# Kernel tuning notes

Hardware: AMD Instinct MI355X
Metric: run time of the kernel (lower is better)

The kernel has to match this reference:

```python
import jax, jax.numpy as jnp
import numpy as np
import math

D_MODEL = 2048
NUM_HEADS = 16
D_HEAD = D_MODEL // NUM_HEADS
ROPE_BASE = 10000.0

def _rope(t, pos):
    # t: [b, h, T, d_head]; standard rotate-half RoPE with base 10000.
    T, d = t.shape[-2], t.shape[-1]
    start = max(pos, 0)  # pos < 0 means training / position 0
    inv_freq = 1.0 / (ROPE_BASE ** (jnp.arange(0, d, 2, dtype=jnp.float32) / d))  # [d/2]
    positions = jnp.arange(start, start + T, dtype=jnp.float32)                   # [T]
    ang = positions[:, None] * inv_freq[None, :]                                  # [T, d/2]
    cos, sin = jnp.cos(ang), jnp.sin(ang)
    x1, x2 = t[..., : d // 2], t[..., d // 2 :]
    return jnp.concatenate([x1 * cos - x2 * sin, x1 * sin + x2 * cos], axis=-1)

def setup_inputs() -> dict:
    key = jax.random.key(0)
    kx, kq, kk, kv, kw = jax.random.split(key, 5)
    s = 1.0 / math.sqrt(D_MODEL)
    return {
        "x": jax.random.normal(kx, (2, 2048, D_MODEL), dtype=jnp.float32),
        "q_out": jax.random.normal(kq, (D_MODEL, D_MODEL), dtype=jnp.float32) * s,
        "k_out": jax.random.normal(kk, (D_MODEL, D_MODEL), dtype=jnp.float32) * s,
        "v_out": jax.random.normal(kv, (D_MODEL, D_MODEL), dtype=jnp.float32) * s,
        "w_out": jax.random.normal(kw, (D_MODEL, D_MODEL), dtype=jnp.float32) * s,
        "pos": 0,
    }

def reference(x, q_out, k_out, v_out, w_out, pos):
    b, t, d = x.shape
    h, dh = NUM_HEADS, D_HEAD

    def heads(y):  # [b, t, d] -> [b, h, t, dh]
        return y.reshape(b, t, h, dh).transpose(0, 2, 1, 3)

    q = _rope(heads(jnp.einsum('btd,de->bte', x, q_out)), pos)
    k = _rope(heads(jnp.einsum('btd,de->bte', x, k_out)), pos)
    v = heads(jnp.einsum('btd,de->bte', x, v_out))

    score = jnp.einsum('bhqd,bhkd->bhqk', q, k) / math.sqrt(dh)
    causal = jnp.triu(jnp.ones((t, t), dtype=bool), k=1)  # True above diagonal -> masked
    score = jnp.where(causal, -jnp.inf, score)
    weights = jax.nn.softmax(score, axis=-1)
    ctx = jnp.einsum('bhqk,bhkd->bhqd', weights, v)        # [b, h, t, dh]
    ctx = ctx.transpose(0, 2, 1, 3).reshape(b, t, d)
    return jnp.einsum('btd,de->bte', ctx, w_out)
```

## Files before the change

kernel.cpp:

```cpp
#include <hip/hip_runtime.h>
#include <hip/hip_bf16.h>
#include <math.h>

#define NH 16
#define DH 128
#define DM 2048
#define BB 2
#define TT 2048

typedef unsigned short u16;
typedef __attribute__((ext_vector_type(8))) __bf16 bf16x8;
typedef __attribute__((ext_vector_type(8))) u16 u16x8;
typedef __attribute__((ext_vector_type(4))) u16 u16x4;
typedef __attribute__((ext_vector_type(4))) float f32x4;

__device__ __forceinline__ float bf2f(u16 a){
  union { unsigned u; float f; } v; v.u = ((unsigned)a) << 16; return v.f;
}
__device__ __forceinline__ u16 f2bf(float f){
  union { float f; unsigned u; } v; v.f = f;
  unsigned r = v.u + 0x7fffu + ((v.u >> 16) & 1u);
  return (u16)(r >> 16);
}
__device__ __forceinline__ __bf16 f2bfh(float f){
  u16 r = f2bf(f); __bf16 h; __builtin_memcpy(&h, &r, 2); return h;
}
__device__ __forceinline__ float bfh2f(__bf16 h){
  u16 r; __builtin_memcpy(&r, &h, 2); return bf2f(r);
}

typedef const __attribute__((address_space(1))) unsigned int* gas_p;
typedef __attribute__((address_space(3))) unsigned int* las_p;
__device__ __forceinline__ void gl_lds16(const u16* g, u16* lds_uniform_base){
  __builtin_amdgcn_global_load_lds((gas_p)(const void*)g,
                                   (las_p)(void*)lds_uniform_base, 16, 0, 0);
}

#define SB() do{ asm volatile("" ::: "memory"); \
                 __builtin_amdgcn_s_barrier();  \
                 asm volatile("" ::: "memory"); }while(0)
#define WAITV8 asm volatile("s_waitcnt vmcnt(8)" ::: "memory")
#define WAITV0 asm volatile("s_waitcnt vmcnt(0)" ::: "memory")

__global__ __launch_bounds__(256)
void prep4(const float* __restrict__ w0, const float* __restrict__ w1,
           const float* __restrict__ w2, const float* __restrict__ x,
           u16* __restrict__ dst, u16* __restrict__ xb){
  __shared__ u16 tile[32][33];
  const int z = blockIdx.z;
  const int tx = threadIdx.x, ty = threadIdx.y;
  if (z == 3){
    const int bid = blockIdx.y * 64 + blockIdx.x;
    const int tid = ty * 32 + tx;
    #pragma unroll
    for (int rep = 0; rep < 2; rep++){
      const int i = bid * 512 + rep * 256 + tid;
      const f32x4 v = *(const f32x4*)(x + (size_t)i * 4);
      u16x4 o;
      #pragma unroll
      for (int j = 0; j < 4; j++) o[j] = f2bf(v[j]);
      *(u16x4*)(xb + (size_t)i * 4) = o;
    }
    return;
  }
  const float* W = (z == 0) ? w0 : (z == 1) ? w1 : w2;
  u16* Wt = dst + (size_t)z * DM * DM;
  const int bx = blockIdx.x * 32, by = blockIdx.y * 32;
  #pragma unroll
  for (int i = 0; i < 32; i += 8)
    tile[ty + i][tx] = f2bf(W[(size_t)(by + ty + i) * DM + bx + tx]);
  __syncthreads();
  #pragma unroll
  for (int i = 0; i < 32; i += 8)
    Wt[(size_t)(bx + ty + i) * DM + by + tx] = tile[tx][ty + i];
}

__global__ __launch_bounds__(256)
void transpose2048(const float* __restrict__ W, u16* __restrict__ Wt){
  __shared__ u16 tile[32][33];
  const int tx = threadIdx.x, ty = threadIdx.y;
  const int bx = blockIdx.x * 32, by = blockIdx.y * 32;
  #pragma unroll
  for (int i = 0; i < 32; i += 8)
    tile[ty + i][tx] = f2bf(W[(size_t)(by + ty + i) * DM + bx + tx]);
  __syncthreads();
  #pragma unroll
  for (int i = 0; i < 32; i += 8)
    Wt[(size_t)(bx + ty + i) * DM + by + tx] = tile[tx][ty + i];
}

__global__ __launch_bounds__(256)
void cvt_f32_bf16(const float* __restrict__ src, u16* __restrict__ dst, int n4){
  const int i = blockIdx.x * 256 + threadIdx.x;
  if (i >= n4) return;
  const f32x4 v = *(const f32x4*)(src + (size_t)i * 4);
  u16x4 o;
  #pragma unroll
  for (int j = 0; j < 4; j++) o[j] = f2bf(v[j]);
  *(u16x4*)(dst + (size_t)i * 4) = o;
}

__global__ __launch_bounds__(256)
void gemm_bt(const u16* __restrict__ A, const u16* __restrict__ Bt_base,
             void* __restrict__ C0, u16* __restrict__ Ck, u16* __restrict__ Cv,
             int mode0){
  __shared__ u16 As[2][128][32];
  __shared__ u16 Bs[2][128][32];
  const int z = blockIdx.z;
  const u16* Bt = Bt_base + (size_t)z * DM * DM;
  void* C = (z == 0) ? C0 : (z == 1) ? (void*)Ck : (void*)Cv;
  const int mode = (z == 0) ? mode0 : (z == 1) ? 3 : 2;

  const int tid = threadIdx.x;
  const int wave = tid >> 6, lane = tid & 63;
  const int wm = wave & 1, wn = wave >> 1;
  const int row16 = lane & 15, quad = lane >> 4;
  const int m0 = blockIdx.x * 128, n0 = blockIdx.y * 128;

  const f32x4 zero = {0.f, 0.f, 0.f, 0.f};
  f32x4 acc[4][4];
  #pragma unroll
  for (int i = 0; i < 4; i++)
    #pragma unroll
    for (int j = 0; j < 4; j++) acc[i][j] = zero;

  const int srow = lane >> 2;
  const int scol = (lane & 3) * 8;

  for (int k0 = 0; k0 < DM; k0 += 64){
    #pragma unroll
    for (int c = 0; c < 2; c++){
      const int rbase = wave * 32 + c * 16;
      const u16* pa = A  + (size_t)(m0 + rbase + srow) * DM + k0 + scol;
      const u16* pb = Bt + (size_t)(n0 + rbase + srow) * DM + k0 + scol;
      gl_lds16(pa,      &As[0][rbase][0]);
      gl_lds16(pa + 32, &As[1][rbase][0]);
      gl_lds16(pb,      &Bs[0][rbase][0]);
      gl_lds16(pb + 32, &Bs[1][rbase][0]);
    }
    __syncthreads();
    #pragma unroll
    for (int buf = 0; buf < 2; buf++){
      bf16x8 af[4], bfr[4];
      #pragma unroll
      for (int mt = 0; mt < 4; mt++)
        af[mt] = *(const bf16x8*)&As[buf][wm * 64 + mt * 16 + row16][quad * 8];
      #pragma unroll
      for (int nt = 0; nt < 4; nt++)
        bfr[nt] = *(const bf16x8*)&Bs[buf][wn * 64 + nt * 16 + row16][quad * 8];
      #pragma unroll
      for (int mt = 0; mt < 4; mt++)
        #pragma unroll
        for (int nt = 0; nt < 4; nt++)
          acc[mt][nt] = __builtin_amdgcn_mfma_f32_16x16x32_bf16(af[mt], bfr[nt], acc[mt][nt], 0, 0, 0);
    }
    __syncthreads();
  }

  #pragma unroll
  for (int mt = 0; mt < 4; mt++){
    #pragma unroll
    for (int nt = 0; nt < 4; nt++){
      #pragma unroll
      for (int r = 0; r < 4; r++){
        const int m = m0 + wm * 64 + mt * 16 + quad * 4 + r;
        const int n = n0 + wn * 64 + nt * 16 + row16;
        const int b = m >> 11, t = m & (TT - 1);
        const int hh = n >> 7, dh = n & (DH - 1);
        if (mode == 1){
          ((u16*)C)[(((size_t)(b * NH + hh) * TT + t) * DH) + dh] = f2bf(acc[mt][nt][r]);
        } else if (mode == 3){
          const int dhs = dh ^ ((t & 7) << 3);
          ((u16*)C)[(((size_t)(b * NH + hh) * TT + t) * DH) + dhs] = f2bf(acc[mt][nt][r]);
        } else if (mode == 2){
          const int ts = (t & 63) ^ ((dh & 7) << 3);
          ((u16*)C)[(((size_t)(b * NH + hh) * 32 + (t >> 6)) * 8192) + dh * 64 + ts] = f2bf(acc[mt][nt][r]);
        } else {
          ((float*)C)[(size_t)m * DM + n] = acc[mt][nt][r];
        }
      }
    }
  }
}

__global__ __launch_bounds__(512)
void gemm8w(const u16* __restrict__ A, const u16* __restrict__ Bt_base,
            void* __restrict__ C0, u16* __restrict__ Ck, u16* __restrict__ Cv,
            int mode0){
  __shared__ u16 As[2][128][64];
  __shared__ u16 Bs[2][256][64];
  const int z = blockIdx.z;
  const u16* Bt = Bt_base + (size_t)z * DM * DM;
  void* C = (z == 0) ? C0 : (z == 1) ? (void*)Ck : (void*)Cv;
  const int mode = (z == 0) ? mode0 : (z == 1) ? 3 : 2;

  const int tid = threadIdx.x;
  const int wave = tid >> 6, lane = tid & 63;
  const int wm = wave >> 2, wn = wave & 3;
  const int row16 = lane & 15, quad = lane >> 4;
  const int m0 = blockIdx.x * 128, n0 = blockIdx.y * 256;

  const f32x4 zero = {0.f, 0.f, 0.f, 0.f};
  f32x4 acc[4][4];
  #pragma unroll
  for (int i = 0; i < 4; i++)
    #pragma unroll
    for (int j = 0; j < 4; j++) acc[i][j] = zero;

  const int sr = lane >> 3;
  const int sc = ((lane & 7) ^ sr) * 8;
  const u16* aB = A  + (size_t)(m0 + wave * 16 + sr) * DM + sc;
  const u16* bB = Bt + (size_t)(n0 + wave * 32 + sr) * DM + sc;

  #define STG8(bf, ku) do{ \
    gl_lds16(aB + (ku),                     &As[bf][wave * 16][0]); \
    gl_lds16(aB + (ku) + (size_t)8 * DM,    &As[bf][wave * 16 + 8][0]); \
    _Pragma("unroll") \
    for (int u = 0; u < 4; u++) \
      gl_lds16(bB + (ku) + (size_t)(u * 8) * DM, &Bs[bf][wave * 32 + u * 8][0]); \
  }while(0)

  STG8(0, 0);
  __syncthreads();

  for (int t = 0; t < 32; ++t){
    const int buf = t & 1;
    if (t < 31) STG8(buf ^ 1, (t + 1) * 64);
    #pragma unroll
    for (int kk = 0; kk < 2; kk++){
      const int pc = ((kk * 4 + quad) ^ (row16 & 7)) * 8;
      bf16x8 af[4], bk[4];
      #pragma unroll
      for (int mt = 0; mt < 4; mt++)
        af[mt] = *(const bf16x8*)&As[buf][wm * 64 + mt * 16 + row16][pc];
      #pragma unroll
      for (int nt = 0; nt < 4; nt++)
        bk[nt] = *(const bf16x8*)&Bs[buf][wn * 64 + nt * 16 + row16][pc];
      __builtin_amdgcn_s_setprio(1);
      #pragma unroll
      for (int mt = 0; mt < 4; mt++)
        #pragma unroll
        for (int nt = 0; nt < 4; nt++)
          acc[mt][nt] = __builtin_amdgcn_mfma_f32_16x16x32_bf16(af[mt], bk[nt], acc[mt][nt], 0, 0, 0);
      __builtin_amdgcn_s_setprio(0);
    }
    __syncthreads();
  }
  #undef STG8

  #pragma unroll
  for (int mt = 0; mt < 4; mt++){
    #pragma unroll
    for (int nt = 0; nt < 4; nt++){
      #pragma unroll
      for (int r = 0; r < 4; r++){
        const int m = m0 + wm * 64 + mt * 16 + quad * 4 + r;
        const int n = n0 + wn * 64 + nt * 16 + row16;
        const int b = m >> 11, t = m & (TT - 1);
        const int hh = n >> 7, dh = n & (DH - 1);
        if (mode == 1){
          ((u16*)C)[(((size_t)(b * NH + hh) * TT + t) * DH) + dh] = f2bf(acc[mt][nt][r]);
        } else if (mode == 3){
          const int dhs = dh ^ ((t & 7) << 3);
          ((u16*)C)[(((size_t)(b * NH + hh) * TT + t) * DH) + dhs] = f2bf(acc[mt][nt][r]);
        } else if (mode == 2){
          const int ts = (t & 63) ^ ((dh & 7) << 3);
          ((u16*)C)[(((size_t)(b * NH + hh) * 32 + (t >> 6)) * 8192) + dh * 64 + ts] = f2bf(acc[mt][nt][r]);
        } else {
          ((float*)C)[(size_t)m * DM + n] = acc[mt][nt][r];
        }
      }
    }
  }
}

__global__ __launch_bounds__(256)
void ropek(u16* __restrict__ kb, const int* __restrict__ posp){
  const int idx = blockIdx.x * 256 + threadIdx.x;
  const int sub = idx & 7;
  const int row = idx >> 3;
  const int t = row & (TT - 1);
  int p0 = *posp; if (p0 < 0) p0 = 0;
  const float tf = (float)(p0 + t);
  const size_t base = (size_t)row * DH + sub * 8;
  u16x8 lo = *(const u16x8*)(kb + base);
  u16x8 hi = *(const u16x8*)(kb + base + 64);
  const int fx = (t & 7) << 3;
  #pragma unroll
  for (int j = 0; j < 8; j++){
    const int pl = (sub * 8 + j) ^ fx;
    const float inv = __expf(-(float)pl * (9.2103403719761836f / 64.f));
    const float a = tf * inv;
    const float sn = __sinf(a), cs = __cosf(a);
    const float k1 = bf2f(lo[j]), k2 = bf2f(hi[j]);
    lo[j] = f2bf(k1 * cs - k2 * sn);
    hi[j] = f2bf(k1 * sn + k2 * cs);
  }
  *(u16x8*)(kb + base)      = lo;
  *(u16x8*)(kb + base + 64) = hi;
}

template<bool MASK>
__device__ __forceinline__ void attn_tile(
    int kt0, int qbase, int wave, int row16, int quad,
    const bf16x8 (&qf)[4],
    u16 (&k_s)[64][128], u16 (&vt_s)[128][64], u16 (&p_s)[4][16][68],
    f32x4 (&o_acc)[8], float (&l_acc)[4])
{
  const float scale = 0.08838834764831845f;
  const f32x4 zero = {0.f, 0.f, 0.f, 0.f};
  const int fx = (row16 & 7) << 3;
  f32x4 s_acc[4];
  #pragma unroll
  for (int nt = 0; nt < 4; nt++) s_acc[nt] = zero;
  __builtin_amdgcn_s_setprio(1);
  #pragma unroll
  for (int st = 0; st < 4; st++)
    #pragma unroll
    for (int nt = 0; nt < 4; nt++){
      const bf16x8 kf = *(const bf16x8*)&k_s[nt * 16 + row16][(st * 32 + quad * 8) ^ fx];
      s_acc[nt] = __builtin_amdgcn_mfma_f32_16x16x32_bf16(qf[st], kf, s_acc[nt], 0, 0, 0);
    }
  __builtin_amdgcn_s_setprio(0);
  #pragma unroll
  for (int r = 0; r < 4; r++){
    float ps = 0.f;
    #pragma unroll
    for (int nt = 0; nt < 4; nt++){
      float p = __expf(s_acc[nt][r] * scale);
      if (MASK){
        const int qr = qbase + quad * 4 + r;
        if (kt0 + nt * 16 + row16 > qr) p = 0.f;
      }
      ps += p;
      p_s[wave][quad * 4 + r][nt * 16 + row16] = f2bf(p);
    }
    l_acc[r] += ps;
  }
  asm volatile("" ::: "memory");

  __builtin_amdgcn_s_setprio(1);
  #pragma unroll
  for (int kk = 0; kk < 2; kk++){
    const bf16x8 pf = *(const bf16x8*)&p_s[wave][row16][kk * 32 + quad * 8];
    #pragma unroll
    for (int nd = 0; nd < 8; nd++){
      const bf16x8 vb = *(const bf16x8*)&vt_s[nd * 16 + row16][(kk * 32 + quad * 8) ^ fx];
      o_acc[nd] = __builtin_amdgcn_mfma_f32_16x16x32_bf16(pf, vb, o_acc[nd], 0, 0, 0);
    }
  }
  __builtin_amdgcn_s_setprio(0);
}

__device__ __forceinline__ void qload_rope(
    const u16* __restrict__ q, size_t bho, int qbase, int p0,
    int row16, int quad, bf16x8 (&qf)[4])
{
  const u16* qp = q + bho + (size_t)(qbase + row16) * DH + quad * 8;
  #pragma unroll
  for (int st = 0; st < 4; st++) qf[st] = *(const bf16x8*)(qp + st * 32);
  const float tf = (float)(p0 + qbase + row16);
  #pragma unroll
  for (int st = 0; st < 2; st++){
    #pragma unroll
    for (int j = 0; j < 8; j++){
      const int dh = st * 32 + quad * 8 + j;
      const float inv = __expf(-(float)dh * (9.2103403719761836f / 64.f));
      const float a = tf * inv;
      const float sn = __sinf(a), cs = __cosf(a);
      const float lo = bfh2f(qf[st][j]), hi = bfh2f(qf[st + 2][j]);
      qf[st][j]     = f2bfh(lo * cs - hi * sn);
      qf[st + 2][j] = f2bfh(lo * sn + hi * cs);
    }
  }
}

__device__ __forceinline__ void owrite(
    u16* __restrict__ ctx, int bh, int qbase, int row16, int quad,
    f32x4 (&o_acc)[8], float (&l_acc)[4])
{
  #pragma unroll
  for (int r = 0; r < 4; r++){
    #pragma unroll
    for (int off = 1; off < 16; off <<= 1) l_acc[r] += __shfl_xor(l_acc[r], off, 64);
  }
  const int b = bh >> 4, h = bh & 15;
  #pragma unroll
  for (int nd = 0; nd < 8; nd++){
    #pragma unroll
    for (int r = 0; r < 4; r++){
      const int qr = qbase + quad * 4 + r;
      const size_t off = ((size_t)b * TT + qr) * DM + h * DH + nd * 16 + row16;
      ctx[off] = f2bf(o_acc[nd][r] / l_acc[r]);
    }
  }
}

__global__ __launch_bounds__(256)
void attn_fwd(const u16* __restrict__ q, const u16* __restrict__ k,
              const u16* __restrict__ vtg, u16* __restrict__ ctx,
              const int* __restrict__ posp){
  __shared__ u16 k_s[2][64][128];
  __shared__ u16 vt_s[2][128][64];
  __shared__ u16 p_s[4][16][68];
  const int tid = threadIdx.x;
  const int wave = tid >> 6, lane = tid & 63;
  const int row16 = lane & 15, quad = lane >> 4;
  const int i = blockIdx.x;
  const int bh = blockIdx.y;
  int p0 = *posp; if (p0 < 0) p0 = 0;
  const size_t bho = (size_t)bh * TT * DH;

  const int qbH = (31 - i) * 64 + wave * 16;
  const int qbL = i * 64 + wave * 16;
  const int nT = 32 - i;

  bf16x8 qfH[4], qfL[4];
  qload_rope(q, bho, qbH, p0, row16, quad, qfH);
  qload_rope(q, bho, qbL, p0, row16, quad, qfL);

  float lH[4] = {0.f, 0.f, 0.f, 0.f}, lL[4] = {0.f, 0.f, 0.f, 0.f};
  const f32x4 zero = {0.f, 0.f, 0.f, 0.f};
  f32x4 oH[8], oL[8];
  #pragma unroll
  for (int j = 0; j < 8; j++){ oH[j] = zero; oL[j] = zero; }

  const int kl_r = lane >> 4, kl_c = (lane & 15) * 8;
  const int vl_r = lane >> 3, vl_c = (lane & 7) * 8;

  #define ASTAGE(t, db) do{ \
    const int kt = (t) * 64; \
    _Pragma("unroll") \
    for (int u = 0; u < 4; u++){ \
      const int rb = wave * 16 + u * 4; \
      gl_lds16(k + bho + (size_t)(kt + rb + kl_r) * DH + kl_c, &k_s[db][rb][0]); \
    } \
    const u16* vpan = vtg + ((size_t)bh * 32 + (t)) * 8192; \
    _Pragma("unroll") \
    for (int u = 0; u < 4; u++){ \
      const int rb = wave * 32 + u * 8; \
      gl_lds16(vpan + (size_t)(rb + vl_r) * 64 + vl_c, &vt_s[db][rb][0]); \
    } \
  }while(0)

  ASTAGE(0, 0);
  for (int t = 0; t < nT; ++t){
    const int db = t & 1;
    if (t + 1 < nT){
      ASTAGE(t + 1, db ^ 1);
      WAITV8;
    } else {
      WAITV0;
    }
    SB();
    if (t < nT - 1)
      attn_tile<false>(t * 64, qbH, wave, row16, quad, qfH, k_s[db], vt_s[db], p_s, oH, lH);
    else
      attn_tile<true >(t * 64, qbH, wave, row16, quad, qfH, k_s[db], vt_s[db], p_s, oH, lH);
    if (t < i)
      attn_tile<false>(t * 64, qbL, wave, row16, quad, qfL, k_s[db], vt_s[db], p_s, oL, lL);
    else if (t == i)
      attn_tile<true >(t * 64, qbL, wave, row16, quad, qfL, k_s[db], vt_s[db], p_s, oL, lL);
    SB();
  }
  #undef ASTAGE

  owrite(ctx, bh, qbH, row16, quad, oH, lH);
  owrite(ctx, bh, qbL, row16, quad, oL, lL);
}

extern "C" void kernel_launch(void* const* d_in, const int* in_sizes, int n_in,
                              void* d_out, int out_size, void* d_ws, size_t ws_size,
                              hipStream_t stream){
  const float* x  = (const float*)d_in[0];
  const float* wq = (const float*)d_in[1];
  const float* wk = (const float*)d_in[2];
  const float* wv = (const float*)d_in[3];
  const float* wo = (const float*)d_in[4];
  const int* pos  = (const int*)d_in[5];

  char* ws = (char*)d_ws;
  const dim3 tg(64, 64), tb(32, 8);

  if (ws_size >= 92274688ull){
    u16* xb  = (u16*)ws;                  u16* cb = xb;
    u16* wt3 = (u16*)(ws + 16777216);
    u16* qb  = (u16*)(ws + 41943040);
    u16* kb  = (u16*)(ws + 58720256);
    u16* vtg = (u16*)(ws + 75497472);

    prep4<<<dim3(64, 64, 4), tb, 0, stream>>>(wq, wk, wv, x, wt3, xb);
    gemm8w<<<dim3(32, 8, 3), 512, 0, stream>>>(xb, wt3, qb, kb, vtg, 1);
    transpose2048<<<tg, tb, 0, stream>>>(wo, wt3);
    ropek<<<2048, 256, 0, stream>>>(kb, pos);
    attn_fwd<<<dim3(16, 32), 256, 0, stream>>>(qb, kb, vtg, cb, pos);
    gemm8w<<<dim3(32, 8, 1), 512, 0, stream>>>(cb, wt3, d_out, 0, 0, 0);
  } else {
    u16* xb  = (u16*)ws;                  u16* cb = xb;
    u16* wt  = (u16*)(ws + 16777216);
    u16* qb  = (u16*)(ws + 25165824);
    u16* kb  = (u16*)(ws + 41943040);
    u16* vtg = (u16*)(ws + 58720256);

    cvt_f32_bf16<<<8192, 256, 0, stream>>>(x, xb, 2097152);
    transpose2048<<<tg, tb, 0, stream>>>(wq, wt);
    gemm_bt<<<dim3(32, 16, 1), 256, 0, stream>>>(xb, wt, qb, 0, 0, 1);
    transpose2048<<<tg, tb, 0, stream>>>(wk, wt);
    gemm_bt<<<dim3(32, 16, 1), 256, 0, stream>>>(xb, wt, kb, 0, 0, 3);
    transpose2048<<<tg, tb, 0, stream>>>(wv, wt);
    gemm_bt<<<dim3(32, 16, 1), 256, 0, stream>>>(xb, wt, vtg, 0, 0, 2);
    ropek<<<2048, 256, 0, stream>>>(kb, pos);
    attn_fwd<<<dim3(16, 32), 256, 0, stream>>>(qb, kb, vtg, cb, pos);
    transpose2048<<<tg, tb, 0, stream>>>(wo, wt);
    gemm_bt<<<dim3(32, 16, 1), 256, 0, stream>>>(cb, wt, d_out, 0, 0, 0);
  }
}
```

Baseline: 422.4 us.

## Use explicit vmcnt waits in QKV GEMM, inline dual Q-RoPE, swap output GEMM

```diff
diff --git a/kernel.cpp b/kernel.cpp
--- a/kernel.cpp
+++ b/kernel.cpp
@@ -40,6 +40,7 @@
                  __builtin_amdgcn_s_barrier();  \
                  asm volatile("" ::: "memory"); }while(0)
 #define WAITV8 asm volatile("s_waitcnt vmcnt(8)" ::: "memory")
+#define WAITV6 asm volatile("s_waitcnt vmcnt(6)" ::: "memory")
 #define WAITV0 asm volatile("s_waitcnt vmcnt(0)" ::: "memory")
 
 __global__ __launch_bounds__(256)
@@ -184,9 +185,9 @@
 }
 
 __global__ __launch_bounds__(512)
-void gemm8w(const u16* __restrict__ A, const u16* __restrict__ Bt_base,
-            void* __restrict__ C0, u16* __restrict__ Ck, u16* __restrict__ Cv,
-            int mode0){
+void gemm8w2(const u16* __restrict__ A, const u16* __restrict__ Bt_base,
+             void* __restrict__ C0, u16* __restrict__ Ck, u16* __restrict__ Cv,
+             int mode0){
   __shared__ u16 As[2][128][64];
   __shared__ u16 Bs[2][256][64];
   const int z = blockIdx.z;
@@ -221,11 +222,16 @@
   }while(0)
 
   STG8(0, 0);
-  __syncthreads();
 
   for (int t = 0; t < 32; ++t){
     const int buf = t & 1;
-    if (t < 31) STG8(buf ^ 1, (t + 1) * 64);
+    if (t < 31){
+      STG8(buf ^ 1, (t + 1) * 64);
+      WAITV6;
+    } else {
+      WAITV0;
+    }
+    SB();
     #pragma unroll
     for (int kk = 0; kk < 2; kk++){
       const int pc = ((kk * 4 + quad) ^ (row16 & 7)) * 8;
@@ -244,7 +250,7 @@
           acc[mt][nt] = __builtin_amdgcn_mfma_f32_16x16x32_bf16(af[mt], bk[nt], acc[mt][nt], 0, 0, 0);
       __builtin_amdgcn_s_setprio(0);
     }
-    __syncthreads();
+    SB();
   }
   #undef STG8
 
@@ -352,29 +358,6 @@
   __builtin_amdgcn_s_setprio(0);
 }
 
-__device__ __forceinline__ void qload_rope(
-    const u16* __restrict__ q, size_t bho, int qbase, int p0,
-    int row16, int quad, bf16x8 (&qf)[4])
-{
-  const u16* qp = q + bho + (size_t)(qbase + row16) * DH + quad * 8;
-  #pragma unroll
-  for (int st = 0; st < 4; st++) qf[st] = *(const bf16x8*)(qp + st * 32);
-  const float tf = (float)(p0 + qbase + row16);
-  #pragma unroll
-  for (int st = 0; st < 2; st++){
-    #pragma unroll
-    for (int j = 0; j < 8; j++){
-      const int dh = st * 32 + quad * 8 + j;
-      const float inv = __expf(-(float)dh * (9.2103403719761836f / 64.f));
-      const float a = tf * inv;
-      const float sn = __sinf(a), cs = __cosf(a);
-      const float lo = bfh2f(qf[st][j]), hi = bfh2f(qf[st + 2][j]);
-      qf[st][j]     = f2bfh(lo * cs - hi * sn);
-      qf[st + 2][j] = f2bfh(lo * sn + hi * cs);
-    }
-  }
-}
-
 __device__ __forceinline__ void owrite(
     u16* __restrict__ ctx, int bh, int qbase, int row16, int quad,
     f32x4 (&o_acc)[8], float (&l_acc)[4])
@@ -416,8 +399,35 @@
   const int nT = 32 - i;
 
   bf16x8 qfH[4], qfL[4];
-  qload_rope(q, bho, qbH, p0, row16, quad, qfH);
-  qload_rope(q, bho, qbL, p0, row16, quad, qfL);
+  {
+    const u16* qpH = q + bho + (size_t)(qbH + row16) * DH + quad * 8;
+    const u16* qpL = q + bho + (size_t)(qbL + row16) * DH + quad * 8;
+    #pragma unroll
+    for (int st = 0; st < 4; st++){
+      qfH[st] = *(const bf16x8*)(qpH + st * 32);
+      qfL[st] = *(const bf16x8*)(qpL + st * 32);
+    }
+    const float tfH = (float)(p0 + qbH + row16);
+    const float tfL = (float)(p0 + qbL + row16);
+    #pragma unroll
+    for (int st = 0; st < 2; st++){
+      #pragma unroll
+      for (int j = 0; j < 8; j++){
+        const int dh = st * 32 + quad * 8 + j;
+        const float inv = __expf(-(float)dh * (9.2103403719761836f / 64.f));
+        float a = tfH * inv;
+        float sn = __sinf(a), cs = __cosf(a);
+        float lo = bfh2f(qfH[st][j]), hi = bfh2f(qfH[st + 2][j]);
+        qfH[st][j]     = f2bfh(lo * cs - hi * sn);
+        qfH[st + 2][j] = f2bfh(lo * sn + hi * cs);
+        a = tfL * inv;
+        sn = __sinf(a); cs = __cosf(a);
+        lo = bfh2f(qfL[st][j]); hi = bfh2f(qfL[st + 2][j]);
+        qfL[st][j]     = f2bfh(lo * cs - hi * sn);
+        qfL[st + 2][j] = f2bfh(lo * sn + hi * cs);
+      }
+    }
+  }
 
   float lH[4] = {0.f, 0.f, 0.f, 0.f}, lL[4] = {0.f, 0.f, 0.f, 0.f};
   const f32x4 zero = {0.f, 0.f, 0.f, 0.f};
@@ -490,11 +500,11 @@
     u16* vtg = (u16*)(ws + 75497472);
 
     prep4<<<dim3(64, 64, 4), tb, 0, stream>>>(wq, wk, wv, x, wt3, xb);
-    gemm8w<<<dim3(32, 8, 3), 512, 0, stream>>>(xb, wt3, qb, kb, vtg, 1);
+    gemm8w2<<<dim3(32, 8, 3), 512, 0, stream>>>(xb, wt3, qb, kb, vtg, 1);
     transpose2048<<<tg, tb, 0, stream>>>(wo, wt3);
     ropek<<<2048, 256, 0, stream>>>(kb, pos);
     attn_fwd<<<dim3(16, 32), 256, 0, stream>>>(qb, kb, vtg, cb, pos);
-    gemm8w<<<dim3(32, 8, 1), 512, 0, stream>>>(cb, wt3, d_out, 0, 0, 0);
+    gemm_bt<<<dim3(32, 16, 1), 256, 0, stream>>>(cb, wt3, d_out, 0, 0, 0);
   } else {
     u16* xb  = (u16*)ws;                  u16* cb = xb;
     u16* wt  = (u16*)(ws + 16777216);
```

Result: no change. 420.8 us (-0.4%).
